# Performance work log

Hardware: AMD Instinct MI355X
Metric: run time of the kernel (lower is better)

The kernel has to match this reference:

```python
import jax, jax.numpy as jnp
import numpy as np

H = 128
NH = 8  # num attention heads


def _ln(x, g, b, eps=1e-5):
    m = x.mean(-1, keepdims=True)
    v = ((x - m) ** 2).mean(-1, keepdims=True)
    return (x - m) / jnp.sqrt(v + eps) * g + b


def _mha(q_in, kv_in, Wqkv, bqkv, Wo, bo):
    # torch nn.MultiheadAttention with packed in_proj, batch=1, eval (no dropout)
    h = q_in.shape[-1]
    hd = h // NH
    Wq, Wk, Wv = Wqkv[:h], Wqkv[h:2 * h], Wqkv[2 * h:]
    bq, bk, bv = bqkv[:h], bqkv[h:2 * h], bqkv[2 * h:]
    q = (q_in @ Wq.T + bq).reshape(-1, NH, hd).transpose(1, 0, 2)   # [nh, Nq, hd]
    k = (kv_in @ Wk.T + bk).reshape(-1, NH, hd).transpose(1, 0, 2)  # [nh, Nk, hd]
    v = (kv_in @ Wv.T + bv).reshape(-1, NH, hd).transpose(1, 0, 2)
    scores = jnp.einsum('hqd,hkd->hqk', q, k) / jnp.sqrt(jnp.asarray(hd, q.dtype))
    attn = jax.nn.softmax(scores, axis=-1)
    out = jnp.einsum('hqk,hkd->hqd', attn, v)                       # [nh, Nq, hd]
    out = out.transpose(1, 0, 2).reshape(-1, h)
    return out @ Wo.T + bo


def setup_inputs() -> dict:
    key = jax.random.key(0)
    ks = jax.random.split(key, 32)
    s = 0.05
    d = {
        'ligand_features': jax.random.normal(ks[0], (512, 128), jnp.float32),
        'pocket_features': jax.random.normal(ks[1], (1024, 128), jnp.float32),
        'ligand_coords': jax.random.uniform(ks[2], (512, 3), jnp.float32) * 20.0,
        'pocket_coords': jax.random.uniform(ks[3], (1024, 3), jnp.float32) * 20.0,
        # projections
        'Wl': jax.random.normal(ks[4], (H, 128), jnp.float32) * s,
        'bl': jnp.zeros((H,), jnp.float32),
        'Wp': jax.random.normal(ks[5], (H, 128), jnp.float32) * s,
        'bp': jnp.zeros((H,), jnp.float32),
        # distance encoder: 1 -> h/4 -> h/2 -> h
        'Wd1': jax.random.normal(ks[6], (H // 4, 1), jnp.float32) * s,
        'bd1': jnp.zeros((H // 4,), jnp.float32),
        'Wd2': jax.random.normal(ks[7], (H // 2, H // 4), jnp.float32) * s,
        'bd2': jnp.zeros((H // 2,), jnp.float32),
        'Wd3': jax.random.normal(ks[8], (H, H // 2), jnp.float32) * s,
        'bd3': jnp.zeros((H,), jnp.float32),
        # gates
        'Wgl': jax.random.normal(ks[9], (H, 2 * H), jnp.float32) * s,
        'bgl': jnp.zeros((H,), jnp.float32),
        'Wgp': jax.random.normal(ks[10], (H, 2 * H), jnp.float32) * s,
        'bgp': jnp.zeros((H,), jnp.float32),
        # shared cross-attention (packed qkv like torch)
        'Wqkv': jax.random.normal(ks[11], (3 * H, H), jnp.float32) * s,
        'bqkv': jnp.zeros((3 * H,), jnp.float32),
        'Wo': jax.random.normal(ks[12], (H, H), jnp.float32) * s,
        'bo': jnp.zeros((H,), jnp.float32),
        # layer norms
        'g_l': jnp.ones((H,), jnp.float32),
        'be_l': jnp.zeros((H,), jnp.float32),
        'g_p': jnp.ones((H,), jnp.float32),
        'be_p': jnp.zeros((H,), jnp.float32),
    }
    return d


def reference(ligand_features, pocket_features, ligand_coords, pocket_coords,
              Wl, bl, Wp, bp, Wd1, bd1, Wd2, bd2, Wd3, bd3,
              Wgl, bgl, Wgp, bgp, Wqkv, bqkv, Wo, bo,
              g_l, be_l, g_p, be_p):
    lig = ligand_features @ Wl.T + bl   # [Nl, H]
    poc = pocket_features @ Wp.T + bp   # [Np, H]

    # pairwise distances [Nl, Np]
    diff = ligand_coords[:, None, :] - pocket_coords[None, :, :]
    dist = jnp.sqrt(jnp.sum(diff * diff, axis=-1))

    # distance encoder MLP applied elementwise -> [Nl, Np, H]
    e = jax.nn.relu(dist[..., None] @ Wd1.T + bd1)
    e = jax.nn.relu(e @ Wd2.T + bd2)
    enc = e @ Wd3.T + bd3
    m = enc.mean(axis=-1)               # [Nl, Np]

    # ligand enhancement: softmax over pocket axis
    sw_l = jax.nn.softmax(-m, axis=-1)          # [Nl, Np]
    agg_l = sw_l @ poc                          # [Nl, H]
    gate_l = jax.nn.sigmoid(jnp.concatenate([lig, agg_l], axis=-1) @ Wgl.T + bgl)
    lig_enh = gate_l * lig + (1.0 - gate_l) * agg_l

    # pocket enhancement: transposed encoding, softmax over ligand axis
    sw_p = jax.nn.softmax(-m.T, axis=-1)        # [Np, Nl]
    agg_p = sw_p @ lig                          # [Np, H]
    gate_p = jax.nn.sigmoid(jnp.concatenate([poc, agg_p], axis=-1) @ Wgp.T + bgp)
    poc_enh = gate_p * poc + (1.0 - gate_p) * agg_p

    lig_att = _mha(lig_enh, poc_enh, Wqkv, bqkv, Wo, bo)
    poc_att = _mha(poc_enh, lig_enh, Wqkv, bqkv, Wo, bo)

    lig_fused = _ln(lig_enh + lig_att, g_l, be_l)
    poc_fused = _ln(poc_enh + poc_att, g_p, be_p)
    return (lig_fused, poc_fused)
```

## Files before the change

### kernel.cpp

```cpp
#include <hip/hip_runtime.h>
#include <math.h>

#define NL 512
#define NP 1024
#define HDIM 128

#define TAB_N 8192
#define DMAX 34.65f

#define WD3M_OFF 0
#define M_OFF    128
#define LIG_OFF  (M_OFF + NL*NP)
#define POC_OFF  (LIG_OFF + NL*HDIM)
#define LENH_OFF (POC_OFF + NP*HDIM)
#define PENH_OFF (LENH_OFF + NL*HDIM)
#define QKVL_OFF (PENH_OFF + NP*HDIM)
#define QKVP_OFF (QKVL_OFF + NL*384)
#define PARTL_OFF (QKVP_OFF + NP*384)
#define PARTP_OFF (PARTL_OFF + 512*8*8*18)
#define TAB_OFF  QKVL_OFF

__device__ __forceinline__ float dot4f(float4 a, float4 b){
  return fmaf(a.x,b.x, fmaf(a.y,b.y, fmaf(a.z,b.z, a.w*b.w)));
}

__global__ __launch_bounds__(128) void prep_kernel(const float* __restrict__ Wd3,
                                                   const float* __restrict__ bd3,
                                                   float* __restrict__ wsw){
  int t = threadIdx.x;
  if (t < 64){
    float s = 0.f;
    #pragma unroll 8
    for (int i = 0; i < 128; i++) s += Wd3[i*64 + t];
    wsw[t] = s * (1.f/128.f);
  } else if (t == 64){
    float s = 0.f;
    for (int i = 0; i < 128; i++) s += bd3[i];
    wsw[64] = s * (1.f/128.f);
  }
}

__global__ __launch_bounds__(128) void proj_kernel(const float* __restrict__ lf, const float* __restrict__ pf,
                                                   const float* __restrict__ Wl, const float* __restrict__ bl,
                                                   const float* __restrict__ Wp, const float* __restrict__ bp,
                                                   float* __restrict__ lig, float* __restrict__ poc){
  int t = threadIdx.x;
  int row0 = blockIdx.x * 4;
  const float* in; const float* W; const float* bias; float* out;
  if (row0 < NL){ in = lf + (size_t)row0*HDIM; W = Wl; bias = bl; out = lig + (size_t)row0*HDIM; }
  else { int r = row0 - NL; in = pf + (size_t)r*HDIM; W = Wp; bias = bp; out = poc + (size_t)r*HDIM; }
  __shared__ float sin[4*HDIM];
  for (int idx = t; idx < 4*HDIM; idx += 128) sin[idx] = in[idx];
  __syncthreads();
  float bv = bias[t];
  float a0 = bv, a1 = bv, a2 = bv, a3 = bv;
  const float4* wr = (const float4*)(W + (size_t)t*HDIM);
  const float4* s0 = (const float4*)(sin);
  const float4* s1 = (const float4*)(sin + HDIM);
  const float4* s2 = (const float4*)(sin + 2*HDIM);
  const float4* s3 = (const float4*)(sin + 3*HDIM);
  #pragma unroll 8
  for (int k = 0; k < 32; k++){
    float4 w = wr[k];
    a0 = fmaf(w.x, s0[k].x, fmaf(w.y, s0[k].y, fmaf(w.z, s0[k].z, fmaf(w.w, s0[k].w, a0))));
    a1 = fmaf(w.x, s1[k].x, fmaf(w.y, s1[k].y, fmaf(w.z, s1[k].z, fmaf(w.w, s1[k].w, a1))));
    a2 = fmaf(w.x, s2[k].x, fmaf(w.y, s2[k].y, fmaf(w.z, s2[k].z, fmaf(w.w, s2[k].w, a2))));
    a3 = fmaf(w.x, s3[k].x, fmaf(w.y, s3[k].y, fmaf(w.z, s3[k].z, fmaf(w.w, s3[k].w, a3))));
  }
  out[t] = a0; out[HDIM + t] = a1; out[2*HDIM + t] = a2; out[3*HDIM + t] = a3;
}

__global__ __launch_bounds__(256) void table_kernel(const float* __restrict__ Wd1, const float* __restrict__ bd1,
                                                    const float* __restrict__ Wd2, const float* __restrict__ bd2,
                                                    const float* __restrict__ wsw, float* __restrict__ tab){
  __shared__ float sWd1[32], sbd1[32], sWd2[2048], sbd2[64], swd3m[64];
  __shared__ float sbd3m;
  int t = threadIdx.x;
  int idx = blockIdx.x * 256 + t;
  if (t < 32){ sWd1[t] = Wd1[t]; sbd1[t] = bd1[t]; }
  if (t >= 32 && t < 96){ sbd2[t-32] = bd2[t-32]; swd3m[t-32] = wsw[t-32]; }
  if (t == 96) sbd3m = wsw[64];
  for (int k = t; k < 2048; k += 256) sWd2[k] = Wd2[k];
  __syncthreads();

  float d = (float)idx * (DMAX / (float)(TAB_N - 1));

  float4 e1q[8];
  const float4* w1q = (const float4*)sWd1;
  const float4* b1q = (const float4*)sbd1;
  #pragma unroll
  for (int k4 = 0; k4 < 8; k4++){
    float4 w = w1q[k4], b = b1q[k4];
    float4 e;
    e.x = fmaxf(fmaf(d, w.x, b.x), 0.f);
    e.y = fmaxf(fmaf(d, w.y, b.y), 0.f);
    e.z = fmaxf(fmaf(d, w.z, b.z), 0.f);
    e.w = fmaxf(fmaf(d, w.w, b.w), 0.f);
    e1q[k4] = e;
  }
  float mv = sbd3m;
  #pragma unroll 4
  for (int j2 = 0; j2 < 64; j2++){
    const float4* wrow = (const float4*)(sWd2 + j2*32);
    float a0 = 0.f, a1 = 0.f, a2 = 0.f, a3 = 0.f;
    #pragma unroll
    for (int k4 = 0; k4 < 8; k4++){
      float4 w = wrow[k4], e = e1q[k4];
      a0 = fmaf(w.x, e.x, a0);
      a1 = fmaf(w.y, e.y, a1);
      a2 = fmaf(w.z, e.z, a2);
      a3 = fmaf(w.w, e.w, a3);
    }
    float e2v = fmaxf(sbd2[j2] + ((a0+a1)+(a2+a3)), 0.f);
    mv = fmaf(swd3m[j2], e2v, mv);
  }
  tab[idx] = mv;
}

__global__ __launch_bounds__(256) void m_lut_kernel(const float* __restrict__ lc, const float* __restrict__ pc,
                                                    const float* __restrict__ tab, float* __restrict__ mout){
  __shared__ float stab[TAB_N];
  int t = threadIdx.x, i = blockIdx.x;
  for (int k = t; k < TAB_N/4; k += 256) ((float4*)stab)[k] = ((const float4*)tab)[k];
  __syncthreads();
  float lx = lc[i*3+0], ly = lc[i*3+1], lz = lc[i*3+2];
  const float4* pc4 = (const float4*)pc;
  float4 A = pc4[3*t], B = pc4[3*t+1], C = pc4[3*t+2];
  const float inv_h = (float)(TAB_N - 1) / DMAX;
  float dxs[4], dys[4], dzs[4];
  dxs[0]=lx-A.x; dys[0]=ly-A.y; dzs[0]=lz-A.z;
  dxs[1]=lx-A.w; dys[1]=ly-B.x; dzs[1]=lz-B.y;
  dxs[2]=lx-B.z; dys[2]=ly-B.w; dzs[2]=lz-C.x;
  dxs[3]=lx-C.y; dys[3]=ly-C.z; dzs[3]=lz-C.w;
  float r[4];
  #pragma unroll
  for (int k = 0; k < 4; k++){
    float d = sqrtf(fmaf(dxs[k],dxs[k], fmaf(dys[k],dys[k], dzs[k]*dzs[k])));
    float x = d * inv_h;
    int i0 = (int)x;
    i0 = (i0 > TAB_N-2) ? (TAB_N-2) : i0;
    float f = x - (float)i0;
    float v0 = stab[i0], v1 = stab[i0+1];
    r[k] = fmaf(f, v1 - v0, v0);
  }
  float4 rv = {r[0], r[1], r[2], r[3]};
  ((float4*)(mout + (size_t)i*NP))[t] = rv;
}

__global__ __launch_bounds__(1024) void agg_gate_fused(const float* __restrict__ msrc,
                                                       const float* __restrict__ lig, const float* __restrict__ poc,
                                                       const float* __restrict__ Wgl, const float* __restrict__ bgl,
                                                       const float* __restrict__ Wgp, const float* __restrict__ bgp,
                                                       float* __restrict__ lenh, float* __restrict__ penh){
  int r = blockIdx.x, t = threadIdx.x;
  __shared__ float w[NP];
  __shared__ float red[32];
  __shared__ float part[1024];
  __shared__ float sx[HDIM], sa[HDIM];
  bool isLig = (r < NL);
  int n = isLig ? NP : NL;

  float x;
  if (isLig)           x = -msrc[(size_t)r*NP + t];
  else if (t < NL)     x = -msrc[(size_t)t*NP + (r - NL)];
  else                 x = -1e30f;

  float v = x;
  #pragma unroll
  for (int off = 32; off; off >>= 1) v = fmaxf(v, __shfl_down(v, off));
  int wid = t >> 6, lane = t & 63;
  if (lane == 0) red[wid] = v;
  __syncthreads();
  if (t == 0){ float mm = red[0]; for (int k = 1; k < 16; k++) mm = fmaxf(mm, red[k]); red[16] = mm; }
  __syncthreads();
  float mx = red[16];

  float e = (t < n) ? __expf(x - mx) : 0.f;
  w[t] = e;
  v = e;
  #pragma unroll
  for (int off = 32; off; off >>= 1) v += __shfl_down(v, off);
  if (lane == 0) red[wid] = v;
  __syncthreads();
  if (t == 0){ float ss = 0.f; for (int k = 0; k < 16; k++) ss += red[k]; red[17] = 1.0f / ss; }
  __syncthreads();
  float inv = red[17];

  int col = t & 127, g = t >> 7;
  const float* src = isLig ? poc : lig;
  int per = n >> 3;
  int j0 = g * per;
  float acc = 0.f;
  #pragma unroll 4
  for (int jj = 0; jj < per; jj++){
    int j = j0 + jj;
    acc = fmaf(w[j], src[(size_t)j*HDIM + col], acc);
  }
  part[t] = acc;
  __syncthreads();
  if (t < 512) part[t] += part[t + 512];
  __syncthreads();
  if (t < 256) part[t] += part[t + 256];
  __syncthreads();
  if (t < 128){
    float a = (part[t] + part[t + 128]) * inv;
    sa[t] = a;
    sx[t] = isLig ? lig[(size_t)r*HDIM + t] : poc[(size_t)(r - NL)*HDIM + t];
  }
  __syncthreads();
  if (t < 128){
    const float* Wg = isLig ? Wgl : Wgp;
    const float* bg = isLig ? bgl : bgp;
    float gacc = bg[t];
    const float4* wr = (const float4*)(Wg + (size_t)t*256);
    const float4* xs = (const float4*)sx;
    const float4* as = (const float4*)sa;
    #pragma unroll 8
    for (int k = 0; k < 32; k++) gacc += dot4f(wr[k], xs[k]);
    #pragma unroll 8
    for (int k = 0; k < 32; k++) gacc += dot4f(wr[32 + k], as[k]);
    gacc = 1.0f / (1.0f + __expf(-gacc));
    float* dst = isLig ? (lenh + (size_t)r*HDIM) : (penh + (size_t)(r - NL)*HDIM);
    dst[t] = fmaf(gacc, sx[t] - sa[t], sa[t]);
  }
}

__global__ __launch_bounds__(384) void qkv_kernel(const float* __restrict__ lenh, const float* __restrict__ penh,
                                                  const float* __restrict__ Wqkv, const float* __restrict__ bqkv,
                                                  float* __restrict__ qkvl, float* __restrict__ qkvp){
  int t = threadIdx.x;
  int row0 = blockIdx.x * 4;
  const float* in; float* out; int rloc;
  if (row0 < NL){ in = lenh + (size_t)row0*HDIM; out = qkvl; rloc = row0; }
  else { rloc = row0 - NL; in = penh + (size_t)rloc*HDIM; out = qkvp; }
  __shared__ float sin[4*HDIM];
  for (int idx = t; idx < 4*HDIM; idx += 384) sin[idx] = in[idx];
  __syncthreads();
  float bv = bqkv[t];
  float a0 = bv, a1 = bv, a2 = bv, a3 = bv;
  const float4* wr = (const float4*)(Wqkv + (size_t)t*HDIM);
  const float4* s0 = (const float4*)(sin);
  const float4* s1 = (const float4*)(sin + HDIM);
  const float4* s2 = (const float4*)(sin + 2*HDIM);
  const float4* s3 = (const float4*)(sin + 3*HDIM);
  #pragma unroll 8
  for (int k = 0; k < 32; k++){
    float4 w = wr[k];
    a0 = fmaf(w.x, s0[k].x, fmaf(w.y, s0[k].y, fmaf(w.z, s0[k].z, fmaf(w.w, s0[k].w, a0))));
    a1 = fmaf(w.x, s1[k].x, fmaf(w.y, s1[k].y, fmaf(w.z, s1[k].z, fmaf(w.w, s1[k].w, a1))));
    a2 = fmaf(w.x, s2[k].x, fmaf(w.y, s2[k].y, fmaf(w.z, s2[k].z, fmaf(w.w, s2[k].w, a2))));
    a3 = fmaf(w.x, s3[k].x, fmaf(w.y, s3[k].y, fmaf(w.z, s3[k].z, fmaf(w.w, s3[k].w, a3))));
  }
  out[(size_t)(rloc+0)*384 + t] = a0;
  out[(size_t)(rloc+1)*384 + t] = a1;
  out[(size_t)(rloc+2)*384 + t] = a2;
  out[(size_t)(rloc+3)*384 + t] = a3;
}

__global__ __launch_bounds__(256) void attn_part(const float* __restrict__ qkvl, const float* __restrict__ qkvp,
                                                 float* __restrict__ partL, float* __restrict__ partP){
  int bx = blockIdx.x;
  int t = threadIdx.x;
  const float* qsrc; const float* kvsrc; int qt, slice; bool isLig;
  if (bx < 256){ isLig = true;  qt = bx >> 3; slice = bx & 7; qsrc = qkvl; kvsrc = qkvp; }
  else { int b2 = bx - 256; isLig = false; qt = b2 >> 2; slice = b2 & 3; qsrc = qkvp; kvsrc = qkvl; }
  int g = t >> 7, tt = t & 127;
  int h = tt >> 4, q = tt & 15;
  int j0 = slice*128 + g*64;

  const float4* qp = (const float4*)(qsrc + (size_t)(qt*16+q)*384 + h*16);
  float4 q0 = qp[0], q1 = qp[1], q2 = qp[2], q3 = qp[3];
  float m = -1e30f, l = 0.f;
  float4 O0 = {0,0,0,0}, O1 = {0,0,0,0}, O2 = {0,0,0,0}, O3 = {0,0,0,0};

  __shared__ float sKV[8192];
  float* myKV = sKV + g*4096;

  for (int tile = 0; tile < 4; tile++){
    int jbase = j0 + tile*16;
    __syncthreads();
    #pragma unroll
    for (int n = 0; n < 8; n++){
      int v4 = tt + n*128;
      int jj = v4 >> 6, c4 = v4 & 63;
      ((float4*)myKV)[(size_t)jj*64 + c4] = *(const float4*)(kvsrc + (size_t)(jbase+jj)*384 + 128 + c4*4);
    }
    __syncthreads();
    float s[16];
    #pragma unroll
    for (int jj = 0; jj < 16; jj++){
      const float4* kk = (const float4*)(myKV + jj*256 + h*16);
      s[jj] = (dot4f(q0, kk[0]) + dot4f(q1, kk[1]) + dot4f(q2, kk[2]) + dot4f(q3, kk[3])) * 0.25f;
    }
    float mt = s[0];
    #pragma unroll
    for (int jj = 1; jj < 16; jj++) mt = fmaxf(mt, s[jj]);
    float mn = fmaxf(m, mt);
    float corr = __expf(m - mn);
    l *= corr;
    O0.x*=corr; O0.y*=corr; O0.z*=corr; O0.w*=corr;
    O1.x*=corr; O1.y*=corr; O1.z*=corr; O1.w*=corr;
    O2.x*=corr; O2.y*=corr; O2.z*=corr; O2.w*=corr;
    O3.x*=corr; O3.y*=corr; O3.z*=corr; O3.w*=corr;
    #pragma unroll
    for (int jj = 0; jj < 16; jj++){
      float p = __expf(s[jj] - mn);
      l += p;
      const float4* vv = (const float4*)(myKV + jj*256 + 128 + h*16);
      O0.x = fmaf(p, vv[0].x, O0.x); O0.y = fmaf(p, vv[0].y, O0.y);
      O0.z = fmaf(p, vv[0].z, O0.z); O0.w = fmaf(p, vv[0].w, O0.w);
      O1.x = fmaf(p, vv[1].x, O1.x); O1.y = fmaf(p, vv[1].y, O1.y);
      O1.z = fmaf(p, vv[1].z, O1.z); O1.w = fmaf(p, vv[1].w, O1.w);
      O2.x = fmaf(p, vv[2].x, O2.x); O2.y = fmaf(p, vv[2].y, O2.y);
      O2.z = fmaf(p, vv[2].z, O2.z); O2.w = fmaf(p, vv[2].w, O2.w);
      O3.x = fmaf(p, vv[3].x, O3.x); O3.y = fmaf(p, vv[3].y, O3.y);
      O3.z = fmaf(p, vv[3].z, O3.z); O3.w = fmaf(p, vv[3].w, O3.w);
    }
    m = mn;
  }

  __syncthreads();
  float* smerge = sKV;
  if (g == 1){
    float* b = smerge + tt*19;
    b[0] = m; b[1] = l;
    b[2]=O0.x; b[3]=O0.y; b[4]=O0.z; b[5]=O0.w;
    b[6]=O1.x; b[7]=O1.y; b[8]=O1.z; b[9]=O1.w;
    b[10]=O2.x; b[11]=O2.y; b[12]=O2.z; b[13]=O2.w;
    b[14]=O3.x; b[15]=O3.y; b[16]=O3.z; b[17]=O3.w;
  }
  __syncthreads();
  if (g == 0){
    const float* b = smerge + tt*19;
    float m1 = b[0], l1 = b[1];
    float M = fmaxf(m, m1);
    float e0 = __expf(m - M), e1 = __expf(m1 - M);
    float L = l*e0 + l1*e1;
    float* dst;
    if (isLig) dst = partL + ((size_t)((qt*16+q)*8 + h)*8 + slice)*18;
    else       dst = partP + ((size_t)((qt*16+q)*8 + h)*4 + slice)*18;
    dst[0] = M; dst[1] = L;
    dst[2]  = O0.x*e0 + b[2]*e1;  dst[3]  = O0.y*e0 + b[3]*e1;
    dst[4]  = O0.z*e0 + b[4]*e1;  dst[5]  = O0.w*e0 + b[5]*e1;
    dst[6]  = O1.x*e0 + b[6]*e1;  dst[7]  = O1.y*e0 + b[7]*e1;
    dst[8]  = O1.z*e0 + b[8]*e1;  dst[9]  = O1.w*e0 + b[9]*e1;
    dst[10] = O2.x*e0 + b[10]*e1; dst[11] = O2.y*e0 + b[11]*e1;
    dst[12] = O2.z*e0 + b[12]*e1; dst[13] = O2.w*e0 + b[13]*e1;
    dst[14] = O3.x*e0 + b[14]*e1; dst[15] = O3.y*e0 + b[15]*e1;
    dst[16] = O3.z*e0 + b[16]*e1; dst[17] = O3.w*e0 + b[17]*e1;
  }
}

__global__ __launch_bounds__(128) void merge_ln(const float* __restrict__ partL, const float* __restrict__ partP,
                                                const float* __restrict__ lenh, const float* __restrict__ penh,
                                                const float* __restrict__ Wo, const float* __restrict__ bo,
                                                const float* __restrict__ g_l, const float* __restrict__ be_l,
                                                const float* __restrict__ g_p, const float* __restrict__ be_p,
                                                float* __restrict__ out){
  int r = blockIdx.x, t = threadIdx.x;
  int h = t >> 4, c = t & 15;
  int ns; const float* base;
  if (r < NL){ ns = 8; base = partL + ((size_t)(r*8 + h))*8*18; }
  else       { ns = 4; base = partP + ((size_t)((r-NL)*8 + h))*4*18; }
  float M = -1e30f;
  for (int s = 0; s < ns; s++) M = fmaxf(M, base[s*18]);
  float Lsum = 0.f, Osum = 0.f;
  for (int s = 0; s < ns; s++){
    float e = __expf(base[s*18] - M);
    Lsum = fmaf(e, base[s*18+1], Lsum);
    Osum = fmaf(e, base[s*18+2+c], Osum);
  }
  __shared__ float satt[HDIM];
  satt[t] = Osum / Lsum;
  __syncthreads();
  float o = bo[t];
  const float4* wr = (const float4*)(Wo + (size_t)t*HDIM);
  const float4* sv = (const float4*)satt;
  #pragma unroll 8
  for (int k = 0; k < 32; k++) o += dot4f(wr[k], sv[k]);
  const float* enh = (r < NL) ? (lenh + (size_t)r*HDIM) : (penh + (size_t)(r-NL)*HDIM);
  float x = enh[t] + o;
  __shared__ float red[HDIM];
  red[t] = x; __syncthreads();
  #pragma unroll
  for (int s = 64; s > 0; s >>= 1){ if (t < s) red[t] += red[t+s]; __syncthreads(); }
  float mu = red[0] * (1.f/128.f); __syncthreads();
  float dx = x - mu;
  red[t] = dx*dx; __syncthreads();
  #pragma unroll
  for (int s = 64; s > 0; s >>= 1){ if (t < s) red[t] += red[t+s]; __syncthreads(); }
  float var = red[0] * (1.f/128.f);
  float y = dx * rsqrtf(var + 1e-5f);
  if (r < NL){
    y = fmaf(y, g_l[t], be_l[t]);
    out[(size_t)r*HDIM + t] = y;
  } else {
    y = fmaf(y, g_p[t], be_p[t]);
    out[(size_t)NL*HDIM + (size_t)(r-NL)*HDIM + t] = y;
  }
}

extern "C" void kernel_launch(void* const* d_in, const int* in_sizes, int n_in,
                              void* d_out, int out_size, void* d_ws, size_t ws_size,
                              hipStream_t stream){
  const float* lf   = (const float*)d_in[0];
  const float* pf   = (const float*)d_in[1];
  const float* lc   = (const float*)d_in[2];
  const float* pc   = (const float*)d_in[3];
  const float* Wl   = (const float*)d_in[4];
  const float* bl   = (const float*)d_in[5];
  const float* Wp   = (const float*)d_in[6];
  const float* bp   = (const float*)d_in[7];
  const float* Wd1  = (const float*)d_in[8];
  const float* bd1  = (const float*)d_in[9];
  const float* Wd2  = (const float*)d_in[10];
  const float* bd2  = (const float*)d_in[11];
  const float* Wd3  = (const float*)d_in[12];
  const float* bd3  = (const float*)d_in[13];
  const float* Wgl  = (const float*)d_in[14];
  const float* bgl  = (const float*)d_in[15];
  const float* Wgp  = (const float*)d_in[16];
  const float* bgp  = (const float*)d_in[17];
  const float* Wqkv = (const float*)d_in[18];
  const float* bqkv = (const float*)d_in[19];
  const float* Wo   = (const float*)d_in[20];
  const float* bo   = (const float*)d_in[21];
  const float* g_l  = (const float*)d_in[22];
  const float* be_l = (const float*)d_in[23];
  const float* g_p  = (const float*)d_in[24];
  const float* be_p = (const float*)d_in[25];

  float* ws  = (float*)d_ws;
  float* out = (float*)d_out;
  float* wsw   = ws + WD3M_OFF;
  float* mws   = ws + M_OFF;
  float* lig   = ws + LIG_OFF;
  float* poc   = ws + POC_OFF;
  float* lenh  = ws + LENH_OFF;
  float* penh  = ws + PENH_OFF;
  float* qkvl  = ws + QKVL_OFF;
  float* qkvp  = ws + QKVP_OFF;
  float* partL = ws + PARTL_OFF;
  float* partP = ws + PARTP_OFF;
  float* tab   = ws + TAB_OFF;

  prep_kernel<<<1, 128, 0, stream>>>(Wd3, bd3, wsw);
  table_kernel<<<TAB_N/256, 256, 0, stream>>>(Wd1, bd1, Wd2, bd2, wsw, tab);
  proj_kernel<<<384, 128, 0, stream>>>(lf, pf, Wl, bl, Wp, bp, lig, poc);
  m_lut_kernel<<<NL, 256, 0, stream>>>(lc, pc, tab, mws);
  agg_gate_fused<<<NL + NP, 1024, 0, stream>>>(mws, lig, poc, Wgl, bgl, Wgp, bgp, lenh, penh);
  qkv_kernel<<<384, 384, 0, stream>>>(lenh, penh, Wqkv, bqkv, qkvl, qkvp);
  attn_part<<<512, 256, 0, stream>>>(qkvl, qkvp, partL, partP);
  merge_ln<<<1536, 128, 0, stream>>>(partL, partP, lenh, penh, Wo, bo, g_l, be_l, g_p, be_p, out);
}
```

Before: 237.0 us.

## Fuse distance-LUT score computation into softmax aggregation and gate kernel

Removes the separate m_lut_kernel and the [Nl,Np] score matrix in global memory. Each aggregation block now loads the 32KB interpolation table into LDS and computes its own row or column of scores from the coordinates, which drops the strided transposed read for pocket rows. The weighted sum is rewritten to float4 loads with a 32-way tree reduction, and the gate matvec is split across 512 threads. The cost is that all 1536 blocks each reload the table and LDS use grows to about 60KB per block, which may lower occupancy.

Result: no change. 233.4 us (-1.5%).

```diff
diff --git a/kernel.cpp b/kernel.cpp
--- a/kernel.cpp
+++ b/kernel.cpp
@@ -117,53 +117,47 @@
   tab[idx] = mv;
 }
 
-__global__ __launch_bounds__(256) void m_lut_kernel(const float* __restrict__ lc, const float* __restrict__ pc,
-                                                    const float* __restrict__ tab, float* __restrict__ mout){
-  __shared__ float stab[TAB_N];
-  int t = threadIdx.x, i = blockIdx.x;
-  for (int k = t; k < TAB_N/4; k += 256) ((float4*)stab)[k] = ((const float4*)tab)[k];
-  __syncthreads();
-  float lx = lc[i*3+0], ly = lc[i*3+1], lz = lc[i*3+2];
-  const float4* pc4 = (const float4*)pc;
-  float4 A = pc4[3*t], B = pc4[3*t+1], C = pc4[3*t+2];
-  const float inv_h = (float)(TAB_N - 1) / DMAX;
-  float dxs[4], dys[4], dzs[4];
-  dxs[0]=lx-A.x; dys[0]=ly-A.y; dzs[0]=lz-A.z;
-  dxs[1]=lx-A.w; dys[1]=ly-B.x; dzs[1]=lz-B.y;
-  dxs[2]=lx-B.z; dys[2]=ly-B.w; dzs[2]=lz-C.x;
-  dxs[3]=lx-C.y; dys[3]=ly-C.z; dzs[3]=lz-C.w;
-  float r[4];
-  #pragma unroll
-  for (int k = 0; k < 4; k++){
-    float d = sqrtf(fmaf(dxs[k],dxs[k], fmaf(dys[k],dys[k], dzs[k]*dzs[k])));
-    float x = d * inv_h;
-    int i0 = (int)x;
-    i0 = (i0 > TAB_N-2) ? (TAB_N-2) : i0;
-    float f = x - (float)i0;
-    float v0 = stab[i0], v1 = stab[i0+1];
-    r[k] = fmaf(f, v1 - v0, v0);
-  }
-  float4 rv = {r[0], r[1], r[2], r[3]};
-  ((float4*)(mout + (size_t)i*NP))[t] = rv;
-}
-
-__global__ __launch_bounds__(1024) void agg_gate_fused(const float* __restrict__ msrc,
+__global__ __launch_bounds__(1024) void agg_gate_fused(const float* __restrict__ lc, const float* __restrict__ pc,
+                                                       const float* __restrict__ tab,
                                                        const float* __restrict__ lig, const float* __restrict__ poc,
                                                        const float* __restrict__ Wgl, const float* __restrict__ bgl,
                                                        const float* __restrict__ Wgp, const float* __restrict__ bgp,
                                                        float* __restrict__ lenh, float* __restrict__ penh){
   int r = blockIdx.x, t = threadIdx.x;
+  __shared__ float stab[TAB_N];
   __shared__ float w[NP];
-  __shared__ float red[32];
-  __shared__ float part[1024];
+  __shared__ float red[20];
+  __shared__ float part[4096];
   __shared__ float sx[HDIM], sa[HDIM];
+  __shared__ float gpart[512];
   bool isLig = (r < NL);
   int n = isLig ? NP : NL;
-
-  float x;
-  if (isLig)           x = -msrc[(size_t)r*NP + t];
-  else if (t < NL)     x = -msrc[(size_t)t*NP + (r - NL)];
-  else                 x = -1e30f;
+  int rloc = isLig ? r : (r - NL);
+
+  for (int k = t; k < TAB_N/4; k += 1024) ((float4*)stab)[k] = ((const float4*)tab)[k];
+
+  const float* ccoord = isLig ? (lc + rloc*3) : (pc + rloc*3);
+  float cx = ccoord[0], cy = ccoord[1], cz = ccoord[2];
+  bool active = t < n;
+  float ox = 0.f, oy = 0.f, oz = 0.f;
+  if (active){
+    const float* oc = isLig ? (pc + t*3) : (lc + t*3);
+    ox = oc[0]; oy = oc[1]; oz = oc[2];
+  }
+  if (t < HDIM) sx[t] = isLig ? lig[(size_t)rloc*HDIM + t] : poc[(size_t)rloc*HDIM + t];
+  __syncthreads();
+
+  float x = -1e30f;
+  if (active){
+    float dx = cx-ox, dy = cy-oy, dz = cz-oz;
+    float d = sqrtf(fmaf(dx,dx, fmaf(dy,dy, dz*dz)));
+    float xf = d * ((float)(TAB_N-1)/DMAX);
+    int i0 = (int)xf;
+    i0 = (i0 > TAB_N-2) ? (TAB_N-2) : i0;
+    float f = xf - (float)i0;
+    float v0 = stab[i0], v1 = stab[i0+1];
+    x = -fmaf(f, v1 - v0, v0);
+  }
 
   float v = x;
   #pragma unroll
@@ -175,7 +169,7 @@
   __syncthreads();
   float mx = red[16];
 
-  float e = (t < n) ? __expf(x - mx) : 0.f;
+  float e = active ? __expf(x - mx) : 0.f;
   w[t] = e;
   v = e;
   #pragma unroll
@@ -186,42 +180,56 @@
   __syncthreads();
   float inv = red[17];
 
-  int col = t & 127, g = t >> 7;
-  const float* src = isLig ? poc : lig;
-  int per = n >> 3;
-  int j0 = g * per;
-  float acc = 0.f;
+  int jg = t >> 5, c4 = t & 31;
+  int per = n >> 5;
+  const float4* src4 = (const float4*)(isLig ? poc : lig);
+  int j0 = jg * per;
+  float4 acc = {0.f, 0.f, 0.f, 0.f};
   #pragma unroll 4
   for (int jj = 0; jj < per; jj++){
     int j = j0 + jj;
-    acc = fmaf(w[j], src[(size_t)j*HDIM + col], acc);
-  }
-  part[t] = acc;
-  __syncthreads();
-  if (t < 512) part[t] += part[t + 512];
-  __syncthreads();
-  if (t < 256) part[t] += part[t + 256];
+    float wj = w[j];
+    float4 sv = src4[(size_t)j*32 + c4];
+    acc.x = fmaf(wj, sv.x, acc.x);
+    acc.y = fmaf(wj, sv.y, acc.y);
+    acc.z = fmaf(wj, sv.z, acc.z);
+    acc.w = fmaf(wj, sv.w, acc.w);
+  }
+  float4* p4 = (float4*)part;
+  p4[jg*32 + c4] = acc;
+  __syncthreads();
+  #pragma unroll
+  for (int s = 16; s >= 1; s >>= 1){
+    if (jg < s){
+      float4 a = p4[jg*32 + c4], b = p4[(jg+s)*32 + c4];
+      a.x += b.x; a.y += b.y; a.z += b.z; a.w += b.w;
+      p4[jg*32 + c4] = a;
+    }
+    __syncthreads();
+  }
+  if (t < 32){
+    float4 a = p4[t];
+    sa[t*4+0] = a.x*inv; sa[t*4+1] = a.y*inv; sa[t*4+2] = a.z*inv; sa[t*4+3] = a.w*inv;
+  }
+  __syncthreads();
+
+  if (t < 512){
+    int col = t & 127, qg = t >> 7;
+    const float* Wg = isLig ? Wgl : Wgp;
+    const float4* wr = (const float4*)(Wg + (size_t)col*256 + qg*64);
+    const float4* inq = (qg < 2) ? ((const float4*)sx + qg*16) : ((const float4*)sa + (qg-2)*16);
+    float g = 0.f;
+    #pragma unroll
+    for (int k = 0; k < 16; k++) g += dot4f(wr[k], inq[k]);
+    gpart[qg*128 + col] = g;
+  }
   __syncthreads();
   if (t < 128){
-    float a = (part[t] + part[t + 128]) * inv;
-    sa[t] = a;
-    sx[t] = isLig ? lig[(size_t)r*HDIM + t] : poc[(size_t)(r - NL)*HDIM + t];
-  }
-  __syncthreads();
-  if (t < 128){
-    const float* Wg = isLig ? Wgl : Wgp;
     const float* bg = isLig ? bgl : bgp;
-    float gacc = bg[t];
-    const float4* wr = (const float4*)(Wg + (size_t)t*256);
-    const float4* xs = (const float4*)sx;
-    const float4* as = (const float4*)sa;
-    #pragma unroll 8
-    for (int k = 0; k < 32; k++) gacc += dot4f(wr[k], xs[k]);
-    #pragma unroll 8
-    for (int k = 0; k < 32; k++) gacc += dot4f(wr[32 + k], as[k]);
-    gacc = 1.0f / (1.0f + __expf(-gacc));
-    float* dst = isLig ? (lenh + (size_t)r*HDIM) : (penh + (size_t)(r - NL)*HDIM);
-    dst[t] = fmaf(gacc, sx[t] - sa[t], sa[t]);
+    float g = bg[t] + ((gpart[t] + gpart[128+t]) + (gpart[256+t] + gpart[384+t]));
+    g = 1.0f / (1.0f + __expf(-g));
+    float* dst = isLig ? (lenh + (size_t)rloc*HDIM) : (penh + (size_t)rloc*HDIM);
+    dst[t] = fmaf(g, sx[t] - sa[t], sa[t]);
   }
 }
 
@@ -433,7 +441,6 @@
   float* ws  = (float*)d_ws;
   float* out = (float*)d_out;
   float* wsw   = ws + WD3M_OFF;
-  float* mws   = ws + M_OFF;
   float* lig   = ws + LIG_OFF;
   float* poc   = ws + POC_OFF;
   float* lenh  = ws + LENH_OFF;
@@ -447,8 +454,7 @@
   prep_kernel<<<1, 128, 0, stream>>>(Wd3, bd3, wsw);
   table_kernel<<<TAB_N/256, 256, 0, stream>>>(Wd1, bd1, Wd2, bd2, wsw, tab);
   proj_kernel<<<384, 128, 0, stream>>>(lf, pf, Wl, bl, Wp, bp, lig, poc);
-  m_lut_kernel<<<NL, 256, 0, stream>>>(lc, pc, tab, mws);
-  agg_gate_fused<<<NL + NP, 1024, 0, stream>>>(mws, lig, poc, Wgl, bgl, Wgp, bgp, lenh, penh);
+  agg_gate_fused<<<NL + NP, 1024, 0, stream>>>(lc, pc, tab, lig, poc, Wgl, bgl, Wgp, bgp, lenh, penh);
   qkv_kernel<<<384, 384, 0, stream>>>(lenh, penh, Wqkv, bqkv, qkvl, qkvp);
   attn_part<<<512, 256, 0, stream>>>(qkvl, qkvp, partL, partP);
   merge_ln<<<1536, 128, 0, stream>>>(partL, partP, lenh, penh, Wo, bo, g_l, be_l, g_p, be_p, out);
```
